# Performance work log

Hardware: AMD Instinct MI355X
Metric: run time of the kernel (lower is better)

Reference implementation:

```python
import jax, jax.numpy as jnp
import numpy as np

N, E, F_IN, H0, H1, H2 = 50000, 800000, 128, 256, 256, 256
NEG = jnp.finfo(jnp.float32).min


def sage_max(x, src, dst, Wl, bl, Wr):
    # PyG SAGEConv(aggr='max'): lin_l(max_j x_j) + lin_r(x_i)
    agg = jax.ops.segment_max(x[src], dst, num_segments=N)  # [N, F]
    agg = jnp.where(agg <= NEG, 0.0, agg)  # isolated nodes -> 0
    return agg @ Wl + bl + x @ Wr


def setup_inputs() -> dict:
    key = jax.random.key(0)
    ks = jax.random.split(key, 16)
    g = lambda k, shp, fan: jax.random.normal(k, shp, jnp.float32) / np.sqrt(fan)
    inp = {
        "x": jax.random.normal(ks[0], (N, F_IN), jnp.float32),
        "edge_index": jax.random.randint(ks[1], (2, E), 0, N, jnp.int64),
        # shared_l1
        "Wl1": g(ks[2], (F_IN, H0), F_IN), "bl1": jnp.zeros((H0,), jnp.float32), "Wr1": g(ks[3], (F_IN, H0), F_IN),
        # shared_l2
        "Wl2": g(ks[4], (H0, H1), H0), "bl2": jnp.zeros((H1,), jnp.float32), "Wr2": g(ks[5], (H0, H1), H0),
        # rtang_l1 + head
        "Wla": g(ks[6], (H1, H2), H1), "bla": jnp.zeros((H2,), jnp.float32), "Wra": g(ks[7], (H1, H2), H1),
        "Wa": g(ks[8], (H2, 1), H2), "ba": jnp.zeros((1,), jnp.float32),
        # movedis_l1 + head
        "Wlm": g(ks[9], (H1, H2), H1), "blm": jnp.zeros((H2,), jnp.float32), "Wrm": g(ks[10], (H1, H2), H1),
        "Wm": g(ks[11], (H2, 1), H2), "bm": jnp.zeros((1,), jnp.float32),
    }
    return inp


def reference(x, edge_index, Wl1, bl1, Wr1, Wl2, bl2, Wr2,
              Wla, bla, Wra, Wa, ba, Wlm, blm, Wrm, Wm, bm):
    src, dst = edge_index[0], edge_index[1]
    h = jax.nn.relu(sage_max(x, src, dst, Wl1, bl1, Wr1))
    h = jax.nn.relu(sage_max(h, src, dst, Wl2, bl2, Wr2))
    rt = jax.nn.relu(sage_max(h, src, dst, Wla, bla, Wra))
    rt = (rt @ Wa + ba).reshape(-1)  # [N]
    mv = jax.nn.relu(sage_max(h, src, dst, Wlm, blm, Wrm))
    mv = (mv @ Wm + bm).reshape(-1)  # [N]
    return (rt, mv)
```

## Files before the change

kernel.cpp:

```cpp
#include <hip/hip_runtime.h>
#include <hip/hip_bf16.h>


#define NN 50000
#define NE 800000
#define HD 256
#define CAP 64

using bf16 = __hip_bfloat16;
typedef float f32x4 __attribute__((ext_vector_type(4)));
typedef short bf16x8 __attribute__((ext_vector_type(8)));

__device__ __forceinline__ void async16(const void* g, void* l) {
    __builtin_amdgcn_global_load_lds(
        (const __attribute__((address_space(1))) unsigned int*)g,
        (__attribute__((address_space(3))) unsigned int*)l, 16, 0, 0);
}

__device__ __forceinline__ unsigned short f2b(float f) {
    bf16 b = __float2bfloat16(f);
    return __builtin_bit_cast(unsigned short, b);
}

__global__ void k_scatter(const int* __restrict__ ei, int* __restrict__ cnt,
                          int* __restrict__ srcp) {
    int e = blockIdx.x * 256 + threadIdx.x;
    if (e < NE) {
        int d = ei[NE + e];
        int slot = atomicAdd(&cnt[d], 1);
        if (slot < CAP) srcp[(d << 6) + slot] = ei[e];
    }
}

__device__ __forceinline__ void pack1(const float* __restrict__ W,
                                      bf16* __restrict__ bt, int idx, int Ktot,
                                      int kofs) {
    int k = idx >> 8, n = idx & 255;
    bt[(size_t)n * Ktot + kofs + k] = __float2bfloat16(W[idx]);
}

#define PREP_CVT_B 6250
#define PREP_PACK_B 1792
#define PREP_INIT_B 391
#define PREP_CNT_B 196
#define PREP_B (PREP_CVT_B + PREP_PACK_B + PREP_INIT_B + PREP_CNT_B)

__global__ void k_prep(const float* __restrict__ x, bf16* __restrict__ xb,
                       const float* __restrict__ Wl1,
                       const float* __restrict__ Wr1,
                       const float* __restrict__ Wl2,
                       const float* __restrict__ Wr2,
                       const float* __restrict__ Wla,
                       const float* __restrict__ Wra,
                       const float* __restrict__ Wlm,
                       const float* __restrict__ Wrm, bf16* __restrict__ Bt1,
                       bf16* __restrict__ Bt2, bf16* __restrict__ Bta,
                       bf16* __restrict__ Btm, float* __restrict__ out,
                       const float* __restrict__ ba,
                       const float* __restrict__ bm, int* __restrict__ cnt) {
    int b = blockIdx.x;
    if (b < PREP_CVT_B) {
        int i = b * 256 + threadIdx.x;
        float4 v = ((const float4*)x)[i];
        ushort4 o;
        o.x = f2b(v.x); o.y = f2b(v.y); o.z = f2b(v.z); o.w = f2b(v.w);
        ((ushort4*)xb)[i] = o;
    } else if (b < PREP_CVT_B + PREP_PACK_B) {
        int idx = (b - PREP_CVT_B) * 256 + threadIdx.x;
        if (idx < 32768) pack1(Wl1, Bt1, idx, 256, 0);
        else if (idx < 65536) pack1(Wr1, Bt1, idx - 32768, 256, 128);
        else if (idx < 131072) pack1(Wl2, Bt2, idx - 65536, 512, 0);
        else if (idx < 196608) pack1(Wr2, Bt2, idx - 131072, 512, 256);
        else if (idx < 262144) pack1(Wla, Bta, idx - 196608, 512, 0);
        else if (idx < 327680) pack1(Wra, Bta, idx - 262144, 512, 256);
        else if (idx < 393216) pack1(Wlm, Btm, idx - 327680, 512, 0);
        else pack1(Wrm, Btm, idx - 393216, 512, 256);
    } else if (b < PREP_CVT_B + PREP_PACK_B + PREP_INIT_B) {
        int i = (b - PREP_CVT_B - PREP_PACK_B) * 256 + threadIdx.x;
        if (i < 2 * NN) out[i] = (i < NN) ? ba[0] : bm[0];
    } else {
        int i = (b - PREP_CVT_B - PREP_PACK_B - PREP_INIT_B) * 256 + threadIdx.x;
        if (i < NN) cnt[i] = 0;
    }
}

template <int EPL>
__global__ __launch_bounds__(256) void k_agg(const bf16* __restrict__ feat,
                                             bf16* __restrict__ agg,
                                             const int* __restrict__ cnt,
                                             const int* __restrict__ srcp) {
    int node = blockIdx.x * 4 + (threadIdx.x >> 6);
    if (node >= NN) return;
    int lane = threadIdx.x & 63;
    int n = min(cnt[node], CAP);
    const int* __restrict__ lst = srcp + (node << 6);
    float m[EPL];
#pragma unroll
    for (int i = 0; i < EPL; ++i) m[i] = __int_as_float(0xff800000);

    auto acc2 = [&](unsigned v, int i0) {
        m[i0] = fmaxf(m[i0], __uint_as_float(v << 16));
        m[i0 + 1] = fmaxf(m[i0 + 1], __uint_as_float(v & 0xffff0000u));
    };

    int e = 0;
    for (; e + 3 < n; e += 4) {
        int sa = lst[e], sb = lst[e + 1], sc = lst[e + 2], sd = lst[e + 3];
        if (EPL == 2) {
            unsigned va = ((const unsigned*)feat)[(size_t)sa * 64 + lane];
            unsigned vb = ((const unsigned*)feat)[(size_t)sb * 64 + lane];
            unsigned vc = ((const unsigned*)feat)[(size_t)sc * 64 + lane];
            unsigned vd = ((const unsigned*)feat)[(size_t)sd * 64 + lane];
            acc2(va, 0); acc2(vb, 0); acc2(vc, 0); acc2(vd, 0);
        } else {
            uint2 va = ((const uint2*)feat)[(size_t)sa * 64 + lane];
            uint2 vb = ((const uint2*)feat)[(size_t)sb * 64 + lane];
            uint2 vc = ((const uint2*)feat)[(size_t)sc * 64 + lane];
            uint2 vd = ((const uint2*)feat)[(size_t)sd * 64 + lane];
            acc2(va.x, 0); acc2(va.y, 2);
            acc2(vb.x, 0); acc2(vb.y, 2);
            acc2(vc.x, 0); acc2(vc.y, 2);
            acc2(vd.x, 0); acc2(vd.y, 2);
        }
    }
    for (; e < n; ++e) {
        int s = lst[e];
        if (EPL == 2) {
            acc2(((const unsigned*)feat)[(size_t)s * 64 + lane], 0);
        } else {
            uint2 v = ((const uint2*)feat)[(size_t)s * 64 + lane];
            acc2(v.x, 0); acc2(v.y, 2);
        }
    }
    unsigned r0 = 0, r1 = 0;
    if (n > 0) {
        r0 = (__float_as_uint(m[0]) >> 16) | (__float_as_uint(m[1]) & 0xffff0000u);
        if (EPL == 4)
            r1 = (__float_as_uint(m[2]) >> 16) | (__float_as_uint(m[3]) & 0xffff0000u);
    }
    if (EPL == 2) {
        ((unsigned*)agg)[(size_t)node * 64 + lane] = r0;
    } else {
        ((uint2*)agg)[(size_t)node * 64 + lane] = make_uint2(r0, r1);
    }
}

__device__ __forceinline__ void gemm_core(const bf16* __restrict__ A0,
                                          const bf16* __restrict__ A1, int F,
                                          int Ktot, const bf16* __restrict__ Bt,
                                          int bm0, int bn0, int t, short* As,
                                          short* Bs, f32x4 (&acc)[4][4]) {
    const int wave = t >> 6;
    const int lane = t & 63;
    const int q = lane >> 4;
    const int c = lane & 15;
    const int wr = (wave >> 1) * 64;
    const int wcl = (wave & 1) * 64;

    for (int k0 = 0; k0 < Ktot; k0 += 64) {
        const bf16* Asrc = (k0 < F) ? A0 : A1;
        const int kk = (k0 < F) ? k0 : k0 - F;
        __syncthreads();
#pragma unroll
        for (int it = 0; it < 4; ++it) {
            int chunk = it * 256 + t;
            int row = chunk >> 3, kc = chunk & 7;
            int kcg = kc ^ (row & 7);
            int grow = bm0 + row;
            if (grow > NN - 1) grow = NN - 1;
            async16(Asrc + (size_t)grow * F + kk + kcg * 8, &As[chunk * 8]);
        }
#pragma unroll
        for (int it = 0; it < 4; ++it) {
            int chunk = it * 256 + t;
            int row = chunk >> 3, kc = chunk & 7;
            int kcg = kc ^ (row & 7);
            async16(Bt + (size_t)(bn0 + row) * Ktot + k0 + kcg * 8,
                    &Bs[chunk * 8]);
        }
        __syncthreads();
#pragma unroll
        for (int ks = 0; ks < 2; ++ks) {
            bf16x8 af[4], bfr[4];
#pragma unroll
            for (int i = 0; i < 4; ++i) {
                int mm = wr + i * 16 + c;
                int ch = (ks * 4 + q) ^ (c & 7);
                af[i] = *(const bf16x8*)&As[mm * 64 + ch * 8];
            }
#pragma unroll
            for (int j = 0; j < 4; ++j) {
                int n = wcl + j * 16 + c;
                int ch = (ks * 4 + q) ^ (c & 7);
                bfr[j] = *(const bf16x8*)&Bs[n * 64 + ch * 8];
            }
#pragma unroll
            for (int i = 0; i < 4; ++i)
#pragma unroll
                for (int j = 0; j < 4; ++j)
                    acc[i][j] = __builtin_amdgcn_mfma_f32_16x16x32_bf16(
                        af[i], bfr[j], acc[i][j], 0, 0, 0);
        }
    }
}

__global__ __launch_bounds__(256) void k_gemm_h(
    const bf16* __restrict__ A0, const bf16* __restrict__ A1, int F, int Ktot,
    const bf16* __restrict__ Bt, const float* __restrict__ bias,
    bf16* __restrict__ Hout) {
    __shared__ __attribute__((aligned(16))) short As[128 * 64];
    __shared__ __attribute__((aligned(16))) short Bs[128 * 64];
    const int t = threadIdx.x;
    const int bm0 = blockIdx.x * 128;
    const int bn0 = blockIdx.y * 128;
    const int wave = t >> 6;
    const int lane = t & 63;
    const int q = lane >> 4;
    const int c = lane & 15;
    const int wr = (wave >> 1) * 64;
    const int wcl = (wave & 1) * 64;

    f32x4 acc[4][4];
#pragma unroll
    for (int i = 0; i < 4; ++i)
#pragma unroll
        for (int j = 0; j < 4; ++j) acc[i][j] = (f32x4){0.f, 0.f, 0.f, 0.f};
    gemm_core(A0, A1, F, Ktot, Bt, bm0, bn0, t, As, Bs, acc);

#pragma unroll
    for (int i = 0; i < 4; ++i)
#pragma unroll
        for (int r = 0; r < 4; ++r) {
            int row = bm0 + wr + i * 16 + q * 4 + r;
            if (row < NN) {
#pragma unroll
                for (int j = 0; j < 4; ++j) {
                    int col = bn0 + wcl + j * 16 + c;
                    float v = acc[i][j][r] + bias[col];
                    v = fmaxf(v, 0.f);
                    Hout[(size_t)row * HD + col] = __float2bfloat16(v);
                }
            }
        }
}

__global__ __launch_bounds__(256) void k_gemm_heads(
    const bf16* __restrict__ A0, const bf16* __restrict__ A1,
    const bf16* __restrict__ Bta, const float* __restrict__ bla,
    const float* __restrict__ Wa, const bf16* __restrict__ Btm,
    const float* __restrict__ blm, const float* __restrict__ Wm,
    float* __restrict__ out) {
    __shared__ __attribute__((aligned(16))) short As[128 * 64];
    __shared__ __attribute__((aligned(16))) short Bs[128 * 64];
    const int t = threadIdx.x;
    const int bm0 = blockIdx.x * 128;
    const int bn0 = blockIdx.y * 128;
    const int z = blockIdx.z;
    const bf16* Bt = z ? Btm : Bta;
    const float* bias = z ? blm : bla;
    const float* Wh = z ? Wm : Wa;
    float* outp = out + (size_t)z * NN;
    const int wave = t >> 6;
    const int lane = t & 63;
    const int q = lane >> 4;
    const int c = lane & 15;
    const int wr = (wave >> 1) * 64;
    const int wcl = (wave & 1) * 64;

    f32x4 acc[4][4];
#pragma unroll
    for (int i = 0; i < 4; ++i)
#pragma unroll
        for (int j = 0; j < 4; ++j) acc[i][j] = (f32x4){0.f, 0.f, 0.f, 0.f};
    gemm_core(A0, A1, 256, 512, Bt, bm0, bn0, t, As, Bs, acc);

#pragma unroll
    for (int i = 0; i < 4; ++i)
#pragma unroll
        for (int r = 0; r < 4; ++r) {
            int row = bm0 + wr + i * 16 + q * 4 + r;
            float p = 0.f;
#pragma unroll
            for (int j = 0; j < 4; ++j) {
                int col = bn0 + wcl + j * 16 + c;
                float v = acc[i][j][r] + bias[col];
                v = fmaxf(v, 0.f);
                p += v * Wh[col];
            }
            p += __shfl_xor(p, 1, 64);
            p += __shfl_xor(p, 2, 64);
            p += __shfl_xor(p, 4, 64);
            p += __shfl_xor(p, 8, 64);
            if (c == 0 && row < NN) atomicAdd(&outp[row], p);
        }
}

extern "C" void kernel_launch(void* const* d_in, const int* in_sizes, int n_in,
                              void* d_out, int out_size, void* d_ws,
                              size_t ws_size, hipStream_t stream) {
    const float* x = (const float*)d_in[0];
    const int* ei = (const int*)d_in[1];
    const float* Wl1 = (const float*)d_in[2];
    const float* bl1 = (const float*)d_in[3];
    const float* Wr1 = (const float*)d_in[4];
    const float* Wl2 = (const float*)d_in[5];
    const float* bl2 = (const float*)d_in[6];
    const float* Wr2 = (const float*)d_in[7];
    const float* Wla = (const float*)d_in[8];
    const float* bla = (const float*)d_in[9];
    const float* Wra = (const float*)d_in[10];
    const float* Wa = (const float*)d_in[11];
    const float* ba = (const float*)d_in[12];
    const float* Wlm = (const float*)d_in[13];
    const float* blm = (const float*)d_in[14];
    const float* Wrm = (const float*)d_in[15];
    const float* Wm = (const float*)d_in[16];
    const float* bm = (const float*)d_in[17];
    float* out = (float*)d_out;

    char* ws = (char*)d_ws;
    size_t off = 0;
    auto alloc = [&](size_t b) {
        void* p = ws + off;
        off = (off + b + 255) & ~(size_t)255;
        return p;
    };
    int* srcp = (int*)alloc((size_t)NN * CAP * 4);
    int* cnt = (int*)alloc((size_t)NN * 4);
    bf16* xb = (bf16*)alloc((size_t)NN * 128 * 2);
    bf16* h1 = (bf16*)alloc((size_t)NN * 256 * 2);
    bf16* h2 = (bf16*)alloc((size_t)NN * 256 * 2);
    bf16* agg = (bf16*)alloc((size_t)NN * 256 * 2);
    bf16* Bt1 = (bf16*)alloc((size_t)256 * 256 * 2);
    bf16* Bt2 = (bf16*)alloc((size_t)256 * 512 * 2);
    bf16* Bta = (bf16*)alloc((size_t)256 * 512 * 2);
    bf16* Btm = (bf16*)alloc((size_t)256 * 512 * 2);
    (void)ws_size; (void)in_sizes; (void)n_in; (void)out_size;

    k_prep<<<PREP_B, 256, 0, stream>>>(x, xb, Wl1, Wr1, Wl2, Wr2, Wla, Wra,
                                       Wlm, Wrm, Bt1, Bt2, Bta, Btm, out, ba,
                                       bm, cnt);
    k_scatter<<<(NE + 255) / 256, 256, 0, stream>>>(ei, cnt, srcp);

    dim3 gg((NN + 127) / 128, 2);
    k_agg<2><<<(NN + 3) / 4, 256, 0, stream>>>(xb, agg, cnt, srcp);
    k_gemm_h<<<gg, 256, 0, stream>>>(agg, xb, 128, 256, Bt1, bl1, h1);
    k_agg<4><<<(NN + 3) / 4, 256, 0, stream>>>(h1, agg, cnt, srcp);
    k_gemm_h<<<gg, 256, 0, stream>>>(agg, h1, 256, 512, Bt2, bl2, h2);
    k_agg<4><<<(NN + 3) / 4, 256, 0, stream>>>(h2, agg, cnt, srcp);
    dim3 gh((NN + 127) / 128, 2, 2);
    k_gemm_heads<<<gh, 256, 0, stream>>>(agg, h2, Bta, bla, Wa, Btm, blm, Wm,
                                         out);
}
```

Measured before the change: 409.6 us.

## Widen GEMM tiles to full 256 columns and replace head atomics with LDS reduction

```diff
diff --git a/kernel.cpp b/kernel.cpp
--- a/kernel.cpp
+++ b/kernel.cpp
@@ -41,9 +41,8 @@
 
 #define PREP_CVT_B 6250
 #define PREP_PACK_B 1792
-#define PREP_INIT_B 391
 #define PREP_CNT_B 196
-#define PREP_B (PREP_CVT_B + PREP_PACK_B + PREP_INIT_B + PREP_CNT_B)
+#define PREP_B (PREP_CVT_B + PREP_PACK_B + PREP_CNT_B)
 
 __global__ void k_prep(const float* __restrict__ x, bf16* __restrict__ xb,
                        const float* __restrict__ Wl1,
@@ -55,9 +54,7 @@
                        const float* __restrict__ Wlm,
                        const float* __restrict__ Wrm, bf16* __restrict__ Bt1,
                        bf16* __restrict__ Bt2, bf16* __restrict__ Bta,
-                       bf16* __restrict__ Btm, float* __restrict__ out,
-                       const float* __restrict__ ba,
-                       const float* __restrict__ bm, int* __restrict__ cnt) {
+                       bf16* __restrict__ Btm, int* __restrict__ cnt) {
     int b = blockIdx.x;
     if (b < PREP_CVT_B) {
         int i = b * 256 + threadIdx.x;
@@ -75,11 +72,8 @@
         else if (idx < 327680) pack1(Wra, Bta, idx - 262144, 512, 256);
         else if (idx < 393216) pack1(Wlm, Btm, idx - 327680, 512, 0);
         else pack1(Wrm, Btm, idx - 393216, 512, 256);
-    } else if (b < PREP_CVT_B + PREP_PACK_B + PREP_INIT_B) {
+    } else {
         int i = (b - PREP_CVT_B - PREP_PACK_B) * 256 + threadIdx.x;
-        if (i < 2 * NN) out[i] = (i < NN) ? ba[0] : bm[0];
-    } else {
-        int i = (b - PREP_CVT_B - PREP_PACK_B - PREP_INIT_B) * 256 + threadIdx.x;
         if (i < NN) cnt[i] = 0;
     }
 }
@@ -145,17 +139,18 @@
     }
 }
 
-__device__ __forceinline__ void gemm_core(const bf16* __restrict__ A0,
-                                          const bf16* __restrict__ A1, int F,
-                                          int Ktot, const bf16* __restrict__ Bt,
-                                          int bm0, int bn0, int t, short* As,
-                                          short* Bs, f32x4 (&acc)[4][4]) {
+__device__ __forceinline__ void gemm_core256(const bf16* __restrict__ A0,
+                                             const bf16* __restrict__ A1, int F,
+                                             int Ktot,
+                                             const bf16* __restrict__ Bt,
+                                             int bm0, int t, short* As,
+                                             short* Bs, f32x4 (&acc)[4][8]) {
     const int wave = t >> 6;
     const int lane = t & 63;
     const int q = lane >> 4;
     const int c = lane & 15;
     const int wr = (wave >> 1) * 64;
-    const int wcl = (wave & 1) * 64;
+    const int wcl = (wave & 1) * 128;
 
     for (int k0 = 0; k0 < Ktot; k0 += 64) {
         const bf16* Asrc = (k0 < F) ? A0 : A1;
@@ -171,62 +166,58 @@
             async16(Asrc + (size_t)grow * F + kk + kcg * 8, &As[chunk * 8]);
         }
 #pragma unroll
-        for (int it = 0; it < 4; ++it) {
+        for (int it = 0; it < 8; ++it) {
             int chunk = it * 256 + t;
             int row = chunk >> 3, kc = chunk & 7;
             int kcg = kc ^ (row & 7);
-            async16(Bt + (size_t)(bn0 + row) * Ktot + k0 + kcg * 8,
-                    &Bs[chunk * 8]);
+            async16(Bt + (size_t)row * Ktot + k0 + kcg * 8, &Bs[chunk * 8]);
         }
         __syncthreads();
 #pragma unroll
         for (int ks = 0; ks < 2; ++ks) {
-            bf16x8 af[4], bfr[4];
-#pragma unroll
-            for (int i = 0; i < 4; ++i) {
-                int mm = wr + i * 16 + c;
-                int ch = (ks * 4 + q) ^ (c & 7);
-                af[i] = *(const bf16x8*)&As[mm * 64 + ch * 8];
-            }
-#pragma unroll
-            for (int j = 0; j < 4; ++j) {
-                int n = wcl + j * 16 + c;
-                int ch = (ks * 4 + q) ^ (c & 7);
-                bfr[j] = *(const bf16x8*)&Bs[n * 64 + ch * 8];
-            }
+            bf16x8 af[4], bfr[8];
+            int ch = (ks * 4 + q) ^ (c & 7);
 #pragma unroll
             for (int i = 0; i < 4; ++i)
-#pragma unroll
-                for (int j = 0; j < 4; ++j)
+                af[i] = *(const bf16x8*)&As[(wr + i * 16 + c) * 64 + ch * 8];
+#pragma unroll
+            for (int j = 0; j < 8; ++j)
+                bfr[j] = *(const bf16x8*)&Bs[(wcl + j * 16 + c) * 64 + ch * 8];
+#pragma unroll
+            for (int i = 0; i < 4; ++i)
+#pragma unroll
+                for (int j = 0; j < 8; ++j)
                     acc[i][j] = __builtin_amdgcn_mfma_f32_16x16x32_bf16(
                         af[i], bfr[j], acc[i][j], 0, 0, 0);
         }
     }
 }
 
-__global__ __launch_bounds__(256) void k_gemm_h(
+__global__ __launch_bounds__(256, 2) void k_gemm_h(
     const bf16* __restrict__ A0, const bf16* __restrict__ A1, int F, int Ktot,
     const bf16* __restrict__ Bt, const float* __restrict__ bias,
     bf16* __restrict__ Hout) {
     __shared__ __attribute__((aligned(16))) short As[128 * 64];
-    __shared__ __attribute__((aligned(16))) short Bs[128 * 64];
+    __shared__ __attribute__((aligned(16))) short Bs[256 * 64];
     const int t = threadIdx.x;
     const int bm0 = blockIdx.x * 128;
-    const int bn0 = blockIdx.y * 128;
     const int wave = t >> 6;
     const int lane = t & 63;
     const int q = lane >> 4;
     const int c = lane & 15;
     const int wr = (wave >> 1) * 64;
-    const int wcl = (wave & 1) * 64;
-
-    f32x4 acc[4][4];
+    const int wcl = (wave & 1) * 128;
+
+    f32x4 acc[4][8];
 #pragma unroll
     for (int i = 0; i < 4; ++i)
 #pragma unroll
-        for (int j = 0; j < 4; ++j) acc[i][j] = (f32x4){0.f, 0.f, 0.f, 0.f};
-    gemm_core(A0, A1, F, Ktot, Bt, bm0, bn0, t, As, Bs, acc);
-
+        for (int j = 0; j < 8; ++j) acc[i][j] = (f32x4){0.f, 0.f, 0.f, 0.f};
+    gemm_core256(A0, A1, F, Ktot, Bt, bm0, t, As, Bs, acc);
+
+    float bcol[8];
+#pragma unroll
+    for (int j = 0; j < 8; ++j) bcol[j] = bias[wcl + j * 16 + c];
 #pragma unroll
     for (int i = 0; i < 4; ++i)
 #pragma unroll
@@ -234,65 +225,87 @@
             int row = bm0 + wr + i * 16 + q * 4 + r;
             if (row < NN) {
 #pragma unroll
-                for (int j = 0; j < 4; ++j) {
-                    int col = bn0 + wcl + j * 16 + c;
-                    float v = acc[i][j][r] + bias[col];
-                    v = fmaxf(v, 0.f);
+                for (int j = 0; j < 8; ++j) {
+                    int col = wcl + j * 16 + c;
+                    float v = fmaxf(acc[i][j][r] + bcol[j], 0.f);
                     Hout[(size_t)row * HD + col] = __float2bfloat16(v);
                 }
             }
         }
 }
 
-__global__ __launch_bounds__(256) void k_gemm_heads(
+__global__ __launch_bounds__(256, 2) void k_gemm_heads(
     const bf16* __restrict__ A0, const bf16* __restrict__ A1,
     const bf16* __restrict__ Bta, const float* __restrict__ bla,
-    const float* __restrict__ Wa, const bf16* __restrict__ Btm,
-    const float* __restrict__ blm, const float* __restrict__ Wm,
+    const float* __restrict__ Wa, const float* __restrict__ ba,
+    const bf16* __restrict__ Btm, const float* __restrict__ blm,
+    const float* __restrict__ Wm, const float* __restrict__ bm,
     float* __restrict__ out) {
     __shared__ __attribute__((aligned(16))) short As[128 * 64];
-    __shared__ __attribute__((aligned(16))) short Bs[128 * 64];
+    __shared__ __attribute__((aligned(16))) short Bs[256 * 64];
     const int t = threadIdx.x;
     const int bm0 = blockIdx.x * 128;
-    const int bn0 = blockIdx.y * 128;
-    const int z = blockIdx.z;
+    const int z = blockIdx.y;
     const bf16* Bt = z ? Btm : Bta;
     const float* bias = z ? blm : bla;
     const float* Wh = z ? Wm : Wa;
+    const float hb = z ? bm[0] : ba[0];
     float* outp = out + (size_t)z * NN;
     const int wave = t >> 6;
     const int lane = t & 63;
     const int q = lane >> 4;
     const int c = lane & 15;
     const int wr = (wave >> 1) * 64;
-    const int wcl = (wave & 1) * 64;
-
-    f32x4 acc[4][4];
+    const int wcl = (wave & 1) * 128;
+
+    f32x4 acc[4][8];
 #pragma unroll
     for (int i = 0; i < 4; ++i)
 #pragma unroll
-        for (int j = 0; j < 4; ++j) acc[i][j] = (f32x4){0.f, 0.f, 0.f, 0.f};
-    gemm_core(A0, A1, 256, 512, Bt, bm0, bn0, t, As, Bs, acc);
-
+        for (int j = 0; j < 8; ++j) acc[i][j] = (f32x4){0.f, 0.f, 0.f, 0.f};
+    gemm_core256(A0, A1, 256, 512, Bt, bm0, t, As, Bs, acc);
+
+    float bcol[8], wcol[8];
+#pragma unroll
+    for (int j = 0; j < 8; ++j) {
+        int col = wcl + j * 16 + c;
+        bcol[j] = bias[col];
+        wcol[j] = Wh[col];
+    }
+    float pr[4][4];
 #pragma unroll
     for (int i = 0; i < 4; ++i)
 #pragma unroll
         for (int r = 0; r < 4; ++r) {
-            int row = bm0 + wr + i * 16 + q * 4 + r;
             float p = 0.f;
 #pragma unroll
-            for (int j = 0; j < 4; ++j) {
-                int col = bn0 + wcl + j * 16 + c;
-                float v = acc[i][j][r] + bias[col];
-                v = fmaxf(v, 0.f);
-                p += v * Wh[col];
-            }
+            for (int j = 0; j < 8; ++j)
+                p += fmaxf(acc[i][j][r] + bcol[j], 0.f) * wcol[j];
             p += __shfl_xor(p, 1, 64);
             p += __shfl_xor(p, 2, 64);
             p += __shfl_xor(p, 4, 64);
             p += __shfl_xor(p, 8, 64);
-            if (c == 0 && row < NN) atomicAdd(&outp[row], p);
-        }
+            pr[i][r] = p;
+        }
+    __syncthreads();
+    float* red = (float*)As;
+    if ((wave & 1) && c == 0) {
+#pragma unroll
+        for (int i = 0; i < 4; ++i)
+#pragma unroll
+            for (int r = 0; r < 4; ++r) red[wr + i * 16 + q * 4 + r] = pr[i][r];
+    }
+    __syncthreads();
+    if (!(wave & 1) && c == 0) {
+#pragma unroll
+        for (int i = 0; i < 4; ++i)
+#pragma unroll
+            for (int r = 0; r < 4; ++r) {
+                int lr = wr + i * 16 + q * 4 + r;
+                int row = bm0 + lr;
+                if (row < NN) outp[row] = pr[i][r] + red[lr] + hb;
+            }
+    }
 }
 
 extern "C" void kernel_launch(void* const* d_in, const int* in_sizes, int n_in,
@@ -338,17 +351,16 @@
     (void)ws_size; (void)in_sizes; (void)n_in; (void)out_size;
 
     k_prep<<<PREP_B, 256, 0, stream>>>(x, xb, Wl1, Wr1, Wl2, Wr2, Wla, Wra,
-                                       Wlm, Wrm, Bt1, Bt2, Bta, Btm, out, ba,
-                                       bm, cnt);
+                                       Wlm, Wrm, Bt1, Bt2, Bta, Btm, cnt);
     k_scatter<<<(NE + 255) / 256, 256, 0, stream>>>(ei, cnt, srcp);
 
-    dim3 gg((NN + 127) / 128, 2);
+    const int GB = (NN + 127) / 128;
     k_agg<2><<<(NN + 3) / 4, 256, 0, stream>>>(xb, agg, cnt, srcp);
-    k_gemm_h<<<gg, 256, 0, stream>>>(agg, xb, 128, 256, Bt1, bl1, h1);
+    k_gemm_h<<<GB, 256, 0, stream>>>(agg, xb, 128, 256, Bt1, bl1, h1);
     k_agg<4><<<(NN + 3) / 4, 256, 0, stream>>>(h1, agg, cnt, srcp);
-    k_gemm_h<<<gg, 256, 0, stream>>>(agg, h1, 256, 512, Bt2, bl2, h2);
+    k_gemm_h<<<GB, 256, 0, stream>>>(agg, h1, 256, 512, Bt2, bl2, h2);
     k_agg<4><<<(NN + 3) / 4, 256, 0, stream>>>(h2, agg, cnt, srcp);
-    dim3 gh((NN + 127) / 128, 2, 2);
-    k_gemm_heads<<<gh, 256, 0, stream>>>(agg, h2, Bta, bla, Wa, Btm, blm, Wm,
-                                         out);
-}
+    dim3 gh(GB, 2);
+    k_gemm_heads<<<gh, 256, 0, stream>>>(agg, h2, Bta, bla, Wa, ba, Btm, blm,
+                                         Wm, bm, out);
+}
```

Result: faster. 369.1 us (-9.9%).
